# Kernel tuning notes

Hardware: AMD Instinct MI355X
Metric: run time of the kernel (lower is better)

## Reference

```python
import jax, jax.numpy as jnp
import numpy as np

D_MODEL = 1024
VOCAB = 32000
NUM_HEADS = 3  # MTP steps
NHEAD = 2      # attention heads per encoder layer
D_FF = 2048    # torch TransformerEncoderLayer default dim_feedforward
EPS_RMS = 1e-8
EPS_LN = 1e-5


def rmsnorm(x):
    rms = jnp.sqrt(jnp.mean(x * x, axis=-1, keepdims=True) + EPS_RMS)
    return x / rms


def layernorm(x, g, b):
    m = jnp.mean(x, axis=-1, keepdims=True)
    v = jnp.mean((x - m) ** 2, axis=-1, keepdims=True)
    return (x - m) / jnp.sqrt(v + EPS_LN) * g + b


def encoder_layer_single_token(x, p):
    # x: (..., d). Self-attention over a length-1 sequence: softmax over one key
    # gives attention weight 1, so attn_out = Wo @ (Wv @ x). Post-norm (torch default).
    v = x @ p['Wv'].T + p['bv']
    attn = v @ p['Wo'].T + p['bo']
    x = layernorm(x + attn, p['ln1_g'], p['ln1_b'])
    ff = jax.nn.relu(x @ p['W1'].T + p['b1']) @ p['W2'].T + p['b2']
    x = layernorm(x + ff, p['ln2_g'], p['ln2_b'])
    return x


def setup_inputs() -> dict:
    key = jax.random.key(0)
    ks = jax.random.split(key, 4)
    token_ids = jax.random.randint(ks[0], (4, 512), 0, VOCAB)
    embed = jax.random.normal(ks[1], (VOCAB, D_MODEL), dtype=jnp.float32) * 0.02
    s = 1.0 / np.sqrt(D_MODEL)
    params = []
    kk = ks[2]
    for k in range(NUM_HEADS):
        kk, *sub = jax.random.split(kk, 10)
        p = {
            'Wmerge': jax.random.normal(sub[0], (D_MODEL, 2 * D_MODEL)) * s,
            'bmerge': jnp.zeros((D_MODEL,)),
            'Wv': jax.random.normal(sub[1], (D_MODEL, D_MODEL)) * s,
            'bv': jnp.zeros((D_MODEL,)),
            'Wo': jax.random.normal(sub[2], (D_MODEL, D_MODEL)) * s,
            'bo': jnp.zeros((D_MODEL,)),
            'W1': jax.random.normal(sub[3], (D_FF, D_MODEL)) * s,
            'b1': jnp.zeros((D_FF,)),
            'W2': jax.random.normal(sub[4], (D_MODEL, D_FF)) * (1.0 / np.sqrt(D_FF)),
            'b2': jnp.zeros((D_MODEL,)),
            'ln1_g': jnp.ones((D_MODEL,)), 'ln1_b': jnp.zeros((D_MODEL,)),
            'ln2_g': jnp.ones((D_MODEL,)), 'ln2_b': jnp.zeros((D_MODEL,)),
        }
        params.append(p)
    # flatten params into dict entries layer{k}_{name}
    out = {'token_ids': token_ids, 'embed': embed}
    for k, p in enumerate(params):
        for name, val in p.items():
            out[f'l{k}_{name}'] = val
    return out


def _forward(token_ids, embed, layers):
    B, T = token_ids.shape
    embeds = embed[token_ids]              # (B, T, d)
    n_pos = T - NUM_HEADS                  # positions i = 0 .. T-NUM_HEADS-1
    # vectorize over i: h_prev starts as h0_seq[:, i, :] for all i at once
    idx = jnp.arange(n_pos)
    h_prev = embeds[:, idx, :]             # (B, P, d)
    logits_list = []
    for k in range(NUM_HEADS):
        p = layers[k]
        tok = embeds[:, idx + (k + 1), :]  # (B, P, d) future token embeds
        merged = jnp.concatenate([rmsnorm(h_prev), rmsnorm(tok)], axis=-1)  # (B,P,2d)
        x = merged @ p['Wmerge'].T + p['bmerge']                            # (B,P,d)
        h_curr = encoder_layer_single_token(x, p)
        logits = h_curr @ embed.T          # tied unembed (B,P,V)
        logits_list.append(logits)
        h_prev = h_curr
    # stack -> (B, P, NUM_HEADS, V) matching torch stack(dim=1) per-position then outer list
    return jnp.stack(logits_list, axis=2)


def reference(token_ids, embed,
              l0_Wmerge, l0_bmerge, l0_Wv, l0_bv, l0_Wo, l0_bo, l0_W1, l0_b1, l0_W2, l0_b2, l0_ln1_g, l0_ln1_b, l0_ln2_g, l0_ln2_b,
              l1_Wmerge, l1_bmerge, l1_Wv, l1_bv, l1_Wo, l1_bo, l1_W1, l1_b1, l1_W2, l1_b2, l1_ln1_g, l1_ln1_b, l1_ln2_g, l1_ln2_b,
              l2_Wmerge, l2_bmerge, l2_Wv, l2_bv, l2_Wo, l2_bo, l2_W1, l2_b1, l2_W2, l2_b2, l2_ln1_g, l2_ln1_b, l2_ln2_g, l2_ln2_b):
    names = ['Wmerge', 'bmerge', 'Wv', 'bv', 'Wo', 'bo', 'W1', 'b1', 'W2', 'b2', 'ln1_g', 'ln1_b', 'ln2_g', 'ln2_b']
    vals = [l0_Wmerge, l0_bmerge, l0_Wv, l0_bv, l0_Wo, l0_bo, l0_W1, l0_b1, l0_W2, l0_b2, l0_ln1_g, l0_ln1_b, l0_ln2_g, l0_ln2_b,
            l1_Wmerge, l1_bmerge, l1_Wv, l1_bv, l1_Wo, l1_bo, l1_W1, l1_b1, l1_W2, l1_b2, l1_ln1_g, l1_ln1_b, l1_ln2_g, l1_ln2_b,
            l2_Wmerge, l2_bmerge, l2_Wv, l2_bv, l2_Wo, l2_bo, l2_W1, l2_b1, l2_W2, l2_b2, l2_ln1_g, l2_ln1_b, l2_ln2_g, l2_ln2_b]
    layers = [dict(zip(names, vals[i * 14:(i + 1) * 14])) for i in range(NUM_HEADS)]
    return _forward(token_ids, embed, layers)
```

## Files before the change

kernel.cpp:

```cpp
#include <hip/hip_runtime.h>


#define NPOS   509
#define MROWS  2036
#define MPAD   2048
#define DMODEL 1024

typedef _Float16 f16;
typedef _Float16 f16x8 __attribute__((ext_vector_type(8)));
typedef _Float16 f16x4 __attribute__((ext_vector_type(4)));
typedef float    f32x4 __attribute__((ext_vector_type(4)));

#define MFMA16(a, b, c) __builtin_amdgcn_mfma_f32_16x16x32_f16(a, b, c, 0, 0, 0)
#define VM0 asm volatile("s_waitcnt vmcnt(0)" ::: "memory")
#define VM2 asm volatile("s_waitcnt vmcnt(2)" ::: "memory")
#define BAR asm volatile("s_barrier" ::: "memory")

__device__ __forceinline__ void gld_lds16(const void* g, void* l) {
  __builtin_amdgcn_global_load_lds(
      (const __attribute__((address_space(1))) void*)g,
      (__attribute__((address_space(3))) void*)l, 16, 0, 0);
}

__global__ __launch_bounds__(256) void conv_f32_f16(const float* __restrict__ src,
                                                    f16* __restrict__ dst, long n) {
  long i = ((long)blockIdx.x * 256 + threadIdx.x) * 8;
  if (i + 8 <= n) {
    float4 a = *(const float4*)(src + i);
    float4 b = *(const float4*)(src + i + 4);
    f16x8 o = {(f16)a.x, (f16)a.y, (f16)a.z, (f16)a.w,
               (f16)b.x, (f16)b.y, (f16)b.z, (f16)b.w};
    *(f16x8*)(dst + i) = o;
  }
}

struct ConvArgs { const float* s[12]; f16* d[12]; long n[12]; };
__global__ __launch_bounds__(256) void conv_many(ConvArgs a) {
  int t = blockIdx.y;
  long i = ((long)blockIdx.x * 256 + threadIdx.x) * 8;
  if (i + 8 <= a.n[t]) {
    const float* src = a.s[t];
    float4 x = *(const float4*)(src + i);
    float4 y = *(const float4*)(src + i + 4);
    f16x8 o = {(f16)x.x, (f16)x.y, (f16)x.z, (f16)x.w,
               (f16)y.x, (f16)y.y, (f16)y.z, (f16)y.w};
    *(f16x8*)(a.d[t] + i) = o;
  }
}

struct TpArgs { const float* s[3]; f16* d[3]; };
__global__ __launch_bounds__(256) void transpose3(TpArgs a) {
  __shared__ float t[32][33];
  int h = blockIdx.z;
  int bx = blockIdx.x * 32, by = blockIdx.y * 32;
  int tx = threadIdx.x & 31, ty = threadIdx.x >> 5;
  const float* src = a.s[h];
  f16* dst = a.d[h];
  #pragma unroll
  for (int r = 0; r < 32; r += 8)
    t[ty + r][tx] = src[(long)(by + ty + r) * 1024 + bx + tx];
  __syncthreads();
  #pragma unroll
  for (int r = 0; r < 32; r += 8)
    dst[(long)(bx + ty + r) * 1024 + by + tx] = (f16)t[tx][ty + r];
}

struct BvoArgs { const float* Wo[3]; const float* bv[3]; const float* bo[3]; float* out[3]; };
__global__ __launch_bounds__(64) void make_bvo3(BvoArgs a) {
  int h = blockIdx.y, r = blockIdx.x, l = threadIdx.x;
  const float* Wo = a.Wo[h];
  const float* bv = a.bv[h];
  float s = 0.0f;
  for (int k = l; k < 1024; k += 64) s += Wo[(long)r * 1024 + k] * bv[k];
  #pragma unroll
  for (int off = 32; off > 0; off >>= 1) s += __shfl_xor(s, off);
  if (l == 0) a.out[h][r] = s + a.bo[h][r];
}

__device__ __forceinline__ float2 block_reduce2(float a, float b) {
  #pragma unroll
  for (int off = 32; off > 0; off >>= 1) {
    a += __shfl_xor(a, off);
    b += __shfl_xor(b, off);
  }
  __shared__ float2 red[4];
  int wv = threadIdx.x >> 6;
  if ((threadIdx.x & 63) == 0) red[wv] = make_float2(a, b);
  __syncthreads();
  float2 r0 = red[0], r1 = red[1], r2 = red[2], r3 = red[3];
  return make_float2(r0.x + r1.x + r2.x + r3.x, r0.y + r1.y + r2.y + r3.y);
}

__global__ __launch_bounds__(256) void merge_rms(const float* __restrict__ hprev,
                                                 const float* __restrict__ embed,
                                                 const int* __restrict__ tok,
                                                 f16* __restrict__ merged, int koff,
                                                 int hsel) {
  int r = blockIdx.x;
  int b = r / NPOS, t = r - b * NPOS;
  int tid = threadIdx.x;
  const float* hrow = (hsel >= 0)
      ? embed + (long)tok[b * 512 + t + hsel] * DMODEL
      : hprev + (long)r * DMODEL;
  float4 hv = ((const float4*)hrow)[tid];
  float4 tv = ((const float4*)(embed + (long)tok[b * 512 + t + koff] * DMODEL))[tid];
  float sh = hv.x * hv.x + hv.y * hv.y + hv.z * hv.z + hv.w * hv.w;
  float st = tv.x * tv.x + tv.y * tv.y + tv.z * tv.z + tv.w * tv.w;
  float2 tot = block_reduce2(sh, st);
  float ih = 1.0f / sqrtf(tot.x * (1.0f / DMODEL) + 1e-8f);
  float it = 1.0f / sqrtf(tot.y * (1.0f / DMODEL) + 1e-8f);
  f16x4 oh = {(f16)(hv.x * ih), (f16)(hv.y * ih), (f16)(hv.z * ih), (f16)(hv.w * ih)};
  f16x4 ot = {(f16)(tv.x * it), (f16)(tv.y * it), (f16)(tv.z * it), (f16)(tv.w * it)};
  *(f16x4*)(merged + (long)r * 2048 + tid * 4) = oh;
  *(f16x4*)(merged + (long)r * 2048 + 1024 + tid * 4) = ot;
}

__global__ __launch_bounds__(256) void add_ln(const float* __restrict__ x,
                                              const float* __restrict__ res,
                                              const float* __restrict__ g,
                                              const float* __restrict__ bb,
                                              float* __restrict__ yf,
                                              f16* __restrict__ yh) {
  int r = blockIdx.x, tid = threadIdx.x;
  float4 a = ((const float4*)(x + (long)r * DMODEL))[tid];
  float4 c = ((const float4*)(res + (long)r * DMODEL))[tid];
  a.x += c.x; a.y += c.y; a.z += c.z; a.w += c.w;
  float s  = a.x + a.y + a.z + a.w;
  float ss = a.x * a.x + a.y * a.y + a.z * a.z + a.w * a.w;
  float2 tot = block_reduce2(s, ss);
  float mean = tot.x * (1.0f / DMODEL);
  float var  = tot.y * (1.0f / DMODEL) - mean * mean;
  float inv  = 1.0f / sqrtf(var + 1e-5f);
  float4 gv = ((const float4*)g)[tid];
  float4 bv = ((const float4*)bb)[tid];
  float y0 = (a.x - mean) * inv * gv.x + bv.x;
  float y1 = (a.y - mean) * inv * gv.y + bv.y;
  float y2 = (a.z - mean) * inv * gv.z + bv.z;
  float y3 = (a.w - mean) * inv * gv.w + bv.w;
  float4 o = {y0, y1, y2, y3};
  ((float4*)(yf + (long)r * DMODEL))[tid] = o;
  f16x4 oh = {(f16)y0, (f16)y1, (f16)y2, (f16)y3};
  *(f16x4*)(yh + (long)r * DMODEL + tid * 4) = oh;
}

template <int HAS_BIAS, int RELU, int WF32, int WF16, int MASK>
__global__ __launch_bounds__(256) void gemm_sm(const f16* __restrict__ A,
                                               const f16* __restrict__ B,
                                               const float* __restrict__ bias,
                                               float* __restrict__ Cf,
                                               f16* __restrict__ Ch,
                                               int K, int N, long ldc, long coff,
                                               int mval, long zsA, long zsB, long zsC) {
  __shared__ __align__(16) f16 sA[3][2048];
  __shared__ __align__(16) f16 sB[3][2048];
  const int tid  = threadIdx.x;
  const int lane = tid & 63, wv = tid >> 6;
  const int wm = wv >> 1, wn = wv & 1;
  const int bm = blockIdx.y, bn = blockIdx.x;
  const int lr = lane & 15, lk = lane >> 4;

  A += (long)blockIdx.z * zsA;
  B += (long)blockIdx.z * zsB;
  Ch += (long)blockIdx.z * zsC;

  const f16* gA = A + ((long)(bm * 64 + (tid >> 2))) * K + (tid & 3) * 8;
  const f16* gB = B + ((long)(bn * 64 + (tid >> 2))) * K + (tid & 3) * 8;

  const int aoff = (wm * 32 + lr) * 32 + lk * 8;
  const int boff = (wn * 32 + lr) * 32 + lk * 8;

  f32x4 acc[2][2] = {};

#define SSTAGE(buf, kt)                                \
  gld_lds16(gA + (long)(kt) * 32, &sA[buf][tid * 8]);  \
  gld_lds16(gB + (long)(kt) * 32, &sB[buf][tid * 8]);

  const int nk = K >> 5;
  SSTAGE(0, 0);
  SSTAGE(1, 1);

  int cur = 0, stg = 2;
  for (int kt = 0; kt < nk; ++kt) {
    if (kt + 1 < nk) { VM2; } else { VM0; }
    BAR;
    if (kt + 2 < nk) { SSTAGE(stg, kt + 2); }
    f16x8 af0 = *(const f16x8*)&sA[cur][aoff];
    f16x8 af1 = *(const f16x8*)&sA[cur][aoff + 512];
    f16x8 bf0 = *(const f16x8*)&sB[cur][boff];
    f16x8 bf1 = *(const f16x8*)&sB[cur][boff + 512];
    acc[0][0] = MFMA16(af0, bf0, acc[0][0]);
    acc[0][1] = MFMA16(af0, bf1, acc[0][1]);
    acc[1][0] = MFMA16(af1, bf0, acc[1][0]);
    acc[1][1] = MFMA16(af1, bf1, acc[1][1]);
    cur = cur == 2 ? 0 : cur + 1;
    stg = stg == 2 ? 0 : stg + 1;
  }
#undef SSTAGE

  const int row0 = bm * 64 + wm * 32 + lk * 4;
  const int col0 = bn * 64 + wn * 32 + lr;
  #pragma unroll
  for (int mi = 0; mi < 2; ++mi) {
    #pragma unroll
    for (int ni = 0; ni < 2; ++ni) {
      int col = col0 + ni * 16;
      float bs = HAS_BIAS ? bias[col] : 0.0f;
      #pragma unroll
      for (int rg = 0; rg < 4; ++rg) {
        int row = row0 + mi * 16 + rg;
        if (!MASK || row < mval) {
          float v = acc[mi][ni][rg] + bs;
          if (RELU) v = v > 0.0f ? v : 0.0f;
          if (WF32) Cf[(long)row * ldc + coff + col] = v;
          if (WF16) Ch[(long)row * N + col] = (f16)v;
        }
      }
    }
  }
}

__global__ __launch_bounds__(512, 2) void gemm256(const f16* __restrict__ A,
                                                  const f16* __restrict__ B,
                                                  float* __restrict__ C,
                                                  int K, long ldc, long coff,
                                                  int mval) {
  __shared__ __align__(16) f16 sA[2][2][8192];
  __shared__ __align__(16) f16 sB[2][2][8192];
  const int tid = threadIdx.x;
  const int lane = tid & 63;
  const int wv = tid >> 6;
  const int wm = wv >> 2, wn = wv & 3;
  const int lr = lane & 15, lk = lane >> 4;

  const int flat = blockIdx.y * 125 + blockIdx.x;
  const int bm = flat & 7, bn = flat >> 3;

  const int srow = tid >> 2;
  const int scol = (tid & 3) * 8;
  const f16* gA = A + (long)(bm * 256 + srow) * K + scol;
  const f16* gB = B + (long)(bn * 256 + srow) * K + scol;
  const long rstep = 128L * (long)K;

  const int aoff = (wm * 128 + lr) * 32 + lk * 8;
  const int boff = (wn * 64  + lr) * 32 + lk * 8;

  f32x4 acc[8][4] = {};

#define STAGE_A(buf, h, ko)                                        \
  gld_lds16(gA + (ko) + (h) * 32, &sA[buf][h][tid * 8]);           \
  gld_lds16(gA + (ko) + (h) * 32 + rstep, &sA[buf][h][tid * 8 + 4096]);
#define STAGE_B(buf, h, ko)                                        \
  gld_lds16(gB + (ko) + (h) * 32, &sB[buf][h][tid * 8]);           \
  gld_lds16(gB + (ko) + (h) * 32 + rstep, &sB[buf][h][tid * 8 + 4096]);
#define VMCNT6  asm volatile("s_waitcnt vmcnt(6)" ::: "memory")

  STAGE_A(0, 0, 0); STAGE_B(0, 0, 0); STAGE_A(0, 1, 0); STAGE_B(0, 1, 0);

  const int nt = K >> 6;
  for (int t = 0; t < nt; ++t) {
    const int cur = t & 1, nxt = cur ^ 1;
    const long kn = (long)((t + 1 < nt) ? (t + 1) : 0) * 64;
    f16x8 af[8], bf[4];

    STAGE_A(nxt, 0, kn);
    VMCNT6;
    BAR;
    #pragma unroll
    for (int mi = 0; mi < 8; ++mi) af[mi] = *(const f16x8*)&sA[cur][0][aoff + mi * 512];
    bf[0] = *(const f16x8*)&sB[cur][0][boff];
    bf[1] = *(const f16x8*)&sB[cur][0][boff + 512];
    __builtin_amdgcn_s_setprio(1);
    #pragma unroll
    for (int mi = 0; mi < 8; ++mi) {
      acc[mi][0] = MFMA16(af[mi], bf[0], acc[mi][0]);
      acc[mi][1] = MFMA16(af[mi], bf[1], acc[mi][1]);
    }
    __builtin_amdgcn_s_setprio(0);
    BAR;

    STAGE_B(nxt, 0, kn);
    BAR;
    bf[2] = *(const f16x8*)&sB[cur][0][boff + 1024];
    bf[3] = *(const f16x8*)&sB[cur][0][boff + 1536];
    __builtin_amdgcn_s_setprio(1);
    #pragma unroll
    for (int mi = 0; mi < 8; ++mi) {
      acc[mi][2] = MFMA16(af[mi], bf[2], acc[mi][2]);
      acc[mi][3] = MFMA16(af[mi], bf[3], acc[mi][3]);
    }
    __builtin_amdgcn_s_setprio(0);
    BAR;

    STAGE_A(nxt, 1, kn);
    VMCNT6;
    BAR;
    #pragma unroll
    for (int mi = 0; mi < 8; ++mi) af[mi] = *(const f16x8*)&sA[cur][1][aoff + mi * 512];
    bf[0] = *(const f16x8*)&sB[cur][1][boff];
    bf[1] = *(const f16x8*)&sB[cur][1][boff + 512];
    __builtin_amdgcn_s_setprio(1);
    #pragma unroll
    for (int mi = 0; mi < 8; ++mi) {
      acc[mi][0] = MFMA16(af[mi], bf[0], acc[mi][0]);
      acc[mi][1] = MFMA16(af[mi], bf[1], acc[mi][1]);
    }
    __builtin_amdgcn_s_setprio(0);
    BAR;

    STAGE_B(nxt, 1, kn);
    BAR;
    bf[2] = *(const f16x8*)&sB[cur][1][boff + 1024];
    bf[3] = *(const f16x8*)&sB[cur][1][boff + 1536];
    __builtin_amdgcn_s_setprio(1);
    #pragma unroll
    for (int mi = 0; mi < 8; ++mi) {
      acc[mi][2] = MFMA16(af[mi], bf[2], acc[mi][2]);
      acc[mi][3] = MFMA16(af[mi], bf[3], acc[mi][3]);
    }
    __builtin_amdgcn_s_setprio(0);
    BAR;
  }
  VM0;

  const int row0 = bm * 256 + wm * 128 + lk * 4;
  const int col0 = bn * 256 + wn * 64 + lr;
  #pragma unroll
  for (int mi = 0; mi < 8; ++mi) {
    #pragma unroll
    for (int ni = 0; ni < 4; ++ni) {
      int col = col0 + ni * 16;
      #pragma unroll
      for (int rg = 0; rg < 4; ++rg) {
        int row = row0 + mi * 16 + rg;
        if (row < mval) C[(long)row * ldc + coff + col] = acc[mi][ni][rg];
      }
    }
  }
#undef STAGE_A
#undef STAGE_B
#undef VMCNT6
}

extern "C" void kernel_launch(void* const* d_in, const int* in_sizes, int n_in,
                              void* d_out, int out_size, void* d_ws, size_t ws_size,
                              hipStream_t stream) {
  const int*   tok   = (const int*)d_in[0];
  const float* embed = (const float*)d_in[1];
  auto P = [&](int k, int j) { return (const float*)d_in[2 + k * 14 + j]; };
  float* out = (float*)d_out;

  char* w = (char*)d_ws;
  auto alloc = [&](size_t bytes) { char* p = w; w += bytes; return p; };
  const size_t MM = (size_t)1024 * 1024;

  f16* embed_h = (f16*)alloc((size_t)32000 * 1024 * 2);
  f16* Wo_all  = (f16*)alloc(3 * MM * 2);
  f16* Wvo_all = (f16*)alloc(3 * MM * 2);
  f16 *Wm_h[3], *W1_h[3], *W2_h[3];
  for (int k = 0; k < 3; ++k) {
    Wm_h[k]  = (f16*)alloc((size_t)1024 * 2048 * 2);
    W1_h[k]  = (f16*)alloc((size_t)2048 * 1024 * 2);
    W2_h[k]  = (f16*)alloc((size_t)1024 * 2048 * 2);
  }
  float* hprev  = (float*)alloc((size_t)MPAD * 1024 * 4);
  f16*   h_h    = (f16*)alloc((size_t)MPAD * 1024 * 2);
  f16*   merged = (f16*)alloc((size_t)MPAD * 2048 * 2);
  float* xf     = (float*)alloc((size_t)MPAD * 1024 * 4);
  f16*   xh     = (f16*)alloc((size_t)MPAD * 1024 * 2);
  f16*   ff1    = (f16*)alloc((size_t)MPAD * 2048 * 2);
  float* t1     = (float*)alloc((size_t)MPAD * 1024 * 4);
  float* bvo    = (float*)alloc(3 * 1024 * 4);
  f16* WvT_all = merged;

  conv_f32_f16<<<16000, 256, 0, stream>>>(embed, embed_h, (long)32000 * 1024);

  ConvArgs ca;
  for (int k = 0; k < 3; ++k) {
    ca.s[k*4+0] = P(k, 0); ca.d[k*4+0] = Wm_h[k];        ca.n[k*4+0] = (long)1024 * 2048;
    ca.s[k*4+1] = P(k, 4); ca.d[k*4+1] = Wo_all + k*MM;  ca.n[k*4+1] = (long)1024 * 1024;
    ca.s[k*4+2] = P(k, 6); ca.d[k*4+2] = W1_h[k];        ca.n[k*4+2] = (long)2048 * 1024;
    ca.s[k*4+3] = P(k, 8); ca.d[k*4+3] = W2_h[k];        ca.n[k*4+3] = (long)1024 * 2048;
  }
  conv_many<<<dim3(1024, 12), 256, 0, stream>>>(ca);

  TpArgs ta;
  for (int k = 0; k < 3; ++k) { ta.s[k] = P(k, 2); ta.d[k] = WvT_all + k * MM; }
  transpose3<<<dim3(32, 32, 3), 256, 0, stream>>>(ta);

  gemm_sm<0, 0, 0, 1, 0><<<dim3(16, 16, 3), 256, 0, stream>>>(
      Wo_all, WvT_all, nullptr, nullptr, Wvo_all, 1024, 1024, 1024L, 0L, 1024,
      (long)MM, (long)MM, (long)MM);

  BvoArgs ba;
  for (int k = 0; k < 3; ++k) {
    ba.Wo[k] = P(k, 4); ba.bv[k] = P(k, 3); ba.bo[k] = P(k, 5); ba.out[k] = bvo + k * 1024;
  }
  make_bvo3<<<dim3(1024, 3), 64, 0, stream>>>(ba);

  for (int k = 0; k < 3; ++k) {
    merge_rms<<<MROWS, 256, 0, stream>>>(hprev, embed, tok, merged, k + 1,
                                         k == 0 ? 0 : -1);
    gemm_sm<1, 0, 1, 1, 0><<<dim3(16, 32), 256, 0, stream>>>(
        merged, Wm_h[k], P(k, 1), xf, xh, 2048, 1024, 1024L, 0L, MROWS, 0L, 0L, 0L);
    gemm_sm<1, 0, 1, 0, 0><<<dim3(16, 32), 256, 0, stream>>>(
        xh, Wvo_all + k * MM, bvo + k * 1024, t1, nullptr, 1024, 1024, 1024L, 0L,
        MROWS, 0L, 0L, 0L);
    add_ln<<<MROWS, 256, 0, stream>>>(xf, t1, P(k, 10), P(k, 11), xf, xh);
    gemm_sm<1, 1, 0, 1, 0><<<dim3(32, 32), 256, 0, stream>>>(
        xh, W1_h[k], P(k, 7), nullptr, ff1, 1024, 2048, 2048L, 0L, MROWS, 0L, 0L, 0L);
    gemm_sm<1, 0, 1, 0, 0><<<dim3(16, 32), 256, 0, stream>>>(
        ff1, W2_h[k], P(k, 9), t1, nullptr, 2048, 1024, 1024L, 0L, MROWS, 0L, 0L, 0L);
    add_ln<<<MROWS, 256, 0, stream>>>(xf, t1, P(k, 12), P(k, 13), hprev, h_h);
    gemm256<<<dim3(125, 8), 512, 0, stream>>>(
        h_h, embed_h, out, 1024, 96000L, (long)k * 32000, MROWS);
  }
}
```

Baseline: 1.125 ms.

## Batch three vocab-projection GEMMs into one launch with 4-stage K pipeline

The three per-head logits GEMMs are deferred and run as a single launch over all three hidden-state buffers, so grid tails and launch gaps are paid once and more blocks are in flight. The GEMM main loop is restructured from a 2-buffer, 64-wide K step with eight barriers per iteration into a 4-stage ring of 32-wide K slices with deeper prefetch (vmcnt 10) and two barriers per iteration. Block indices are also remapped so that each XCD group handles contiguous M tiles, which should improve L2 reuse of the A rows. The cost is an extra 2x hidden-state buffer and hardcoded K/M/ldc constants.

```diff
diff --git a/kernel.cpp b/kernel.cpp
--- a/kernel.cpp
+++ b/kernel.cpp
@@ -12,9 +12,10 @@
 typedef float    f32x4 __attribute__((ext_vector_type(4)));
 
 #define MFMA16(a, b, c) __builtin_amdgcn_mfma_f32_16x16x32_f16(a, b, c, 0, 0, 0)
-#define VM0 asm volatile("s_waitcnt vmcnt(0)" ::: "memory")
-#define VM2 asm volatile("s_waitcnt vmcnt(2)" ::: "memory")
-#define BAR asm volatile("s_barrier" ::: "memory")
+#define VM0  asm volatile("s_waitcnt vmcnt(0)" ::: "memory")
+#define VM2  asm volatile("s_waitcnt vmcnt(2)" ::: "memory")
+#define VM10 asm volatile("s_waitcnt vmcnt(10)" ::: "memory")
+#define BAR  asm volatile("s_barrier" ::: "memory")
 
 __device__ __forceinline__ void gld_lds16(const void* g, void* l) {
   __builtin_amdgcn_global_load_lds(
@@ -219,13 +220,12 @@
   }
 }
 
-__global__ __launch_bounds__(512, 2) void gemm256(const f16* __restrict__ A,
-                                                  const f16* __restrict__ B,
-                                                  float* __restrict__ C,
-                                                  int K, long ldc, long coff,
-                                                  int mval) {
-  __shared__ __align__(16) f16 sA[2][2][8192];
-  __shared__ __align__(16) f16 sB[2][2][8192];
+__global__ __launch_bounds__(512, 2) void gemm256x(const f16* __restrict__ A,
+                                                   const f16* __restrict__ B,
+                                                   float* __restrict__ C) {
+  __shared__ __align__(16) f16 sA[4][8192];
+  __shared__ __align__(16) f16 sB[4][8192];
+  const int K = 1024;
   const int tid = threadIdx.x;
   const int lane = tid & 63;
   const int wv = tid >> 6;
@@ -233,7 +233,9 @@
   const int lr = lane & 15, lk = lane >> 4;
 
   const int flat = blockIdx.y * 125 + blockIdx.x;
-  const int bm = flat & 7, bn = flat >> 3;
+  const int xcd = flat & 7, idx = flat >> 3;
+  const int bm = xcd * 3 + (idx % 3);
+  const int bn = idx / 3;
 
   const int srow = tid >> 2;
   const int scol = (tid & 3) * 8;
@@ -246,29 +248,30 @@
 
   f32x4 acc[8][4] = {};
 
-#define STAGE_A(buf, h, ko)                                        \
-  gld_lds16(gA + (ko) + (h) * 32, &sA[buf][h][tid * 8]);           \
-  gld_lds16(gA + (ko) + (h) * 32 + rstep, &sA[buf][h][tid * 8 + 4096]);
-#define STAGE_B(buf, h, ko)                                        \
-  gld_lds16(gB + (ko) + (h) * 32, &sB[buf][h][tid * 8]);           \
-  gld_lds16(gB + (ko) + (h) * 32 + rstep, &sB[buf][h][tid * 8 + 4096]);
-#define VMCNT6  asm volatile("s_waitcnt vmcnt(6)" ::: "memory")
-
-  STAGE_A(0, 0, 0); STAGE_B(0, 0, 0); STAGE_A(0, 1, 0); STAGE_B(0, 1, 0);
-
-  const int nt = K >> 6;
+#define STG_A(s, kt)                                            \
+  gld_lds16(gA + (long)(kt) * 32, &sA[s][tid * 8]);             \
+  gld_lds16(gA + (long)(kt) * 32 + rstep, &sA[s][tid * 8 + 4096]);
+#define STG_B(s, kt)                                            \
+  gld_lds16(gB + (long)(kt) * 32, &sB[s][tid * 8]);             \
+  gld_lds16(gB + (long)(kt) * 32 + rstep, &sB[s][tid * 8 + 4096]);
+
+  STG_A(0, 0); STG_B(0, 0);
+  STG_A(1, 1); STG_B(1, 1);
+  STG_A(2, 2); STG_B(2, 2);
+
+  const int nt = 32;
   for (int t = 0; t < nt; ++t) {
-    const int cur = t & 1, nxt = cur ^ 1;
-    const long kn = (long)((t + 1 < nt) ? (t + 1) : 0) * 64;
+    const int cur = t & 3, pre = (t + 3) & 3;
+    const int kt = (t + 3 < nt) ? (t + 3) : 0;
     f16x8 af[8], bf[4];
 
-    STAGE_A(nxt, 0, kn);
-    VMCNT6;
+    STG_A(pre, kt);
+    VM10;
     BAR;
     #pragma unroll
-    for (int mi = 0; mi < 8; ++mi) af[mi] = *(const f16x8*)&sA[cur][0][aoff + mi * 512];
-    bf[0] = *(const f16x8*)&sB[cur][0][boff];
-    bf[1] = *(const f16x8*)&sB[cur][0][boff + 512];
+    for (int mi = 0; mi < 8; ++mi) af[mi] = *(const f16x8*)&sA[cur][aoff + mi * 512];
+    bf[0] = *(const f16x8*)&sB[cur][boff];
+    bf[1] = *(const f16x8*)&sB[cur][boff + 512];
     __builtin_amdgcn_s_setprio(1);
     #pragma unroll
     for (int mi = 0; mi < 8; ++mi) {
@@ -276,12 +279,10 @@
       acc[mi][1] = MFMA16(af[mi], bf[1], acc[mi][1]);
     }
     __builtin_amdgcn_s_setprio(0);
-    BAR;
-
-    STAGE_B(nxt, 0, kn);
-    BAR;
-    bf[2] = *(const f16x8*)&sB[cur][0][boff + 1024];
-    bf[3] = *(const f16x8*)&sB[cur][0][boff + 1536];
+
+    STG_B(pre, kt);
+    bf[2] = *(const f16x8*)&sB[cur][boff + 1024];
+    bf[3] = *(const f16x8*)&sB[cur][boff + 1536];
     __builtin_amdgcn_s_setprio(1);
     #pragma unroll
     for (int mi = 0; mi < 8; ++mi) {
@@ -290,39 +291,12 @@
     }
     __builtin_amdgcn_s_setprio(0);
     BAR;
-
-    STAGE_A(nxt, 1, kn);
-    VMCNT6;
-    BAR;
-    #pragma unroll
-    for (int mi = 0; mi < 8; ++mi) af[mi] = *(const f16x8*)&sA[cur][1][aoff + mi * 512];
-    bf[0] = *(const f16x8*)&sB[cur][1][boff];
-    bf[1] = *(const f16x8*)&sB[cur][1][boff + 512];
-    __builtin_amdgcn_s_setprio(1);
-    #pragma unroll
-    for (int mi = 0; mi < 8; ++mi) {
-      acc[mi][0] = MFMA16(af[mi], bf[0], acc[mi][0]);
-      acc[mi][1] = MFMA16(af[mi], bf[1], acc[mi][1]);
-    }
-    __builtin_amdgcn_s_setprio(0);
-    BAR;
-
-    STAGE_B(nxt, 1, kn);
-    BAR;
-    bf[2] = *(const f16x8*)&sB[cur][1][boff + 1024];
-    bf[3] = *(const f16x8*)&sB[cur][1][boff + 1536];
-    __builtin_amdgcn_s_setprio(1);
-    #pragma unroll
-    for (int mi = 0; mi < 8; ++mi) {
-      acc[mi][2] = MFMA16(af[mi], bf[2], acc[mi][2]);
-      acc[mi][3] = MFMA16(af[mi], bf[3], acc[mi][3]);
-    }
-    __builtin_amdgcn_s_setprio(0);
-    BAR;
   }
   VM0;
 
-  const int row0 = bm * 256 + wm * 128 + lk * 4;
+  const int head = bm >> 3;
+  const long coff = (long)head * 32000;
+  const int row0 = (bm & 7) * 256 + wm * 128 + lk * 4;
   const int col0 = bn * 256 + wn * 64 + lr;
   #pragma unroll
   for (int mi = 0; mi < 8; ++mi) {
@@ -332,13 +306,12 @@
       #pragma unroll
       for (int rg = 0; rg < 4; ++rg) {
         int row = row0 + mi * 16 + rg;
-        if (row < mval) C[(long)row * ldc + coff + col] = acc[mi][ni][rg];
+        if (row < MROWS) C[(long)row * 96000 + coff + col] = acc[mi][ni][rg];
       }
     }
   }
-#undef STAGE_A
-#undef STAGE_B
-#undef VMCNT6
+#undef STG_A
+#undef STG_B
 }
 
 extern "C" void kernel_launch(void* const* d_in, const int* in_sizes, int n_in,
@@ -363,7 +336,7 @@
     W2_h[k]  = (f16*)alloc((size_t)1024 * 2048 * 2);
   }
   float* hprev  = (float*)alloc((size_t)MPAD * 1024 * 4);
-  f16*   h_h    = (f16*)alloc((size_t)MPAD * 1024 * 2);
+  f16*   h_all  = (f16*)alloc((size_t)3 * MPAD * 1024 * 2);
   f16*   merged = (f16*)alloc((size_t)MPAD * 2048 * 2);
   float* xf     = (float*)alloc((size_t)MPAD * 1024 * 4);
   f16*   xh     = (f16*)alloc((size_t)MPAD * 1024 * 2);
@@ -410,8 +383,9 @@
         xh, W1_h[k], P(k, 7), nullptr, ff1, 1024, 2048, 2048L, 0L, MROWS, 0L, 0L, 0L);
     gemm_sm<1, 0, 1, 0, 0><<<dim3(16, 32), 256, 0, stream>>>(
         ff1, W2_h[k], P(k, 9), t1, nullptr, 2048, 1024, 1024L, 0L, MROWS, 0L, 0L, 0L);
-    add_ln<<<MROWS, 256, 0, stream>>>(xf, t1, P(k, 12), P(k, 13), hprev, h_h);
-    gemm256<<<dim3(125, 8), 512, 0, stream>>>(
-        h_h, embed_h, out, 1024, 96000L, (long)k * 32000, MROWS);
-  }
-}
+    add_ln<<<MROWS, 256, 0, stream>>>(xf, t1, P(k, 12), P(k, 13), hprev,
+                                      h_all + (size_t)k * MPAD * 1024);
+  }
+
+  gemm256x<<<dim3(125, 24), 512, 0, stream>>>(h_all, embed_h, out);
+}
```

New measurement: 1.037 ms. 7.9% less time.
